# Kernel optimization log

Hardware: AMD Instinct MI355X
Metric: run time of the kernel (lower is better)

Reference implementation:

```python
import jax, jax.numpy as jnp
import numpy as np

KERNEL = 31
GROUPS = 8
EPS = 1e-5


def mha1d(x, Wq, Wk, Wv, rel):
    """Sliding-window multi-head attention (MutliHeadAttention1D).
    x: [b, s, in_f]; Wq/Wk/Wv: [out_f, in_f] (torch Linear layout); rel: [1, out_f, KERNEL].
    Returns (out [b, s, out_f], attn [b, s, GROUPS, KERNEL])."""
    b, s, _ = x.shape
    out_f = Wq.shape[0]
    d = out_f // GROUPS
    pad = (KERNEL - 1) // 2
    xp = jnp.pad(x, ((0, 0), (pad, pad), (0, 0)))
    q = jnp.einsum('bsf,of->bso', x, Wq)          # [b, s, out_f]
    k = jnp.einsum('bsf,of->bso', xp, Wk)         # [b, s+2*pad, out_f]
    v = jnp.einsum('bsf,of->bso', xp, Wv)
    # unfold: window index [s, KERNEL]
    idx = jnp.arange(s)[:, None] + jnp.arange(KERNEL)[None, :]
    kw = jnp.swapaxes(k[:, idx], 2, 3) + rel       # [b, s, out_f, KERNEL]
    vw = jnp.swapaxes(v[:, idx], 2, 3)             # [b, s, out_f, KERNEL]
    kw = kw.reshape(b, s, GROUPS, d, KERNEL)
    vw = vw.reshape(b, s, GROUPS, d, KERNEL)
    qh = q.reshape(b, s, GROUPS, d, 1)
    energy = jnp.sum(qh * kw, axis=-2, keepdims=True)   # [b, s, g, 1, K]
    attn = jax.nn.softmax(energy, axis=-1)               # [b, s, g, 1, K]
    out = jnp.sum(attn * vw, axis=-1).reshape(b, s, out_f)
    return out, attn[:, :, :, 0, :]


def layer_norm(x, g, b):
    mu = jnp.mean(x, axis=-1, keepdims=True)
    var = jnp.mean(jnp.square(x - mu), axis=-1, keepdims=True)
    return (x - mu) / jnp.sqrt(var + EPS) * g + b


def setup_inputs() -> dict:
    key = jax.random.key(0)
    ks = jax.random.split(key, 20)
    in_f, mc, out_f = 229, 48, 88
    d = {}
    d['spec'] = jax.random.normal(ks[0], (8, 8192, in_f), dtype=jnp.float32)
    # onset attention block (in 229 -> 48)
    d['Wq1'] = jax.random.normal(ks[1], (mc, in_f), dtype=jnp.float32) * 0.1
    d['Wk1'] = jax.random.normal(ks[2], (mc, in_f), dtype=jnp.float32) * 0.1
    d['Wv1'] = jax.random.normal(ks[3], (mc, in_f), dtype=jnp.float32) * 0.1
    d['rel1'] = jax.random.normal(ks[4], (1, mc, KERNEL), dtype=jnp.float32)
    d['ln1_g'] = jnp.ones((mc,), jnp.float32)
    d['ln1_b'] = jnp.zeros((mc,), jnp.float32)
    d['Wo'] = jax.random.normal(ks[5], (out_f, mc), dtype=jnp.float32) * 0.1
    d['bo'] = jnp.zeros((out_f,), jnp.float32)
    # frame attention block (in 48+88=136 -> 48)
    in2 = mc + out_f
    d['Wq2'] = jax.random.normal(ks[6], (mc, in2), dtype=jnp.float32) * 0.1
    d['Wk2'] = jax.random.normal(ks[7], (mc, in2), dtype=jnp.float32) * 0.1
    d['Wv2'] = jax.random.normal(ks[8], (mc, in2), dtype=jnp.float32) * 0.1
    d['rel2'] = jax.random.normal(ks[9], (1, mc, KERNEL), dtype=jnp.float32)
    d['ln2_g'] = jnp.ones((mc,), jnp.float32)
    d['ln2_b'] = jnp.zeros((mc,), jnp.float32)
    d['Wf'] = jax.random.normal(ks[10], (out_f, mc), dtype=jnp.float32) * 0.1
    d['bf'] = jnp.zeros((out_f,), jnp.float32)
    return d


def reference(spec, Wq1, Wk1, Wv1, rel1, ln1_g, ln1_b, Wo, bo,
              Wq2, Wk2, Wv2, rel2, ln2_g, ln2_b, Wf, bf):
    x, a = mha1d(spec, Wq1, Wk1, Wv1, rel1)
    x = layer_norm(x, ln1_g, ln1_b)
    onset_pred = jax.nn.sigmoid(jnp.einsum('bsm,om->bso', x, Wo) + bo)
    x = jnp.concatenate((onset_pred, x), axis=-1)
    x, _ = mha1d(x, Wq2, Wk2, Wv2, rel2)
    x = layer_norm(x, ln2_g, ln2_b)
    frame_pred = jax.nn.sigmoid(jnp.einsum('bsm,om->bso', x, Wf) + bf)
    return frame_pred, onset_pred, a
```

## Files before the change

### kernel.cpp

```cpp
#include <hip/hip_runtime.h>
#include <math.h>

namespace {

constexpr int B_   = 8;
constexpr int S_   = 8192;
constexpr int NROW = B_ * S_;
constexpr int MC   = 48;
constexpr int OF   = 88;
constexpr int KW   = 31;
constexpr int F1   = 229;
constexpr int F2   = 136;

typedef __attribute__((ext_vector_type(8))) short bf16x8;
typedef __attribute__((ext_vector_type(4))) float f32x4;

__device__ inline unsigned short f2bf(float v) {
    unsigned u = __float_as_uint(v);
    unsigned r = (u + 0x7FFFu + ((u >> 16) & 1u)) >> 16;
    return (unsigned short)r;
}
__device__ inline float bf2f(unsigned short b) {
    return __uint_as_float((unsigned)b << 16);
}
__device__ inline unsigned pack2(unsigned short a, unsigned short b) {
    return (unsigned)a | ((unsigned)b << 16);
}

__global__ void wprep_kernel(const float* __restrict__ Wq,
                             const float* __restrict__ Wk,
                             const float* __restrict__ Wv,
                             int K, int nch, unsigned short* __restrict__ out) {
    int idx = blockIdx.x * 256 + threadIdx.x;
    int kpad = nch * 32;
    int total = 144 * kpad;
    if (idx >= total) return;
    int oc = idx / kpad;
    int kg = idx - oc * kpad;
    int c  = kg >> 5, kk = kg & 31;
    float val = 0.f;
    if (kg < K) {
        const float* W = (oc < 48) ? Wq : (oc < 96 ? Wk : Wv);
        int ocl = (oc < 48) ? oc : (oc < 96 ? oc - 48 : oc - 96);
        val = W[ocl * K + kg];
    }
    unsigned short h = f2bf(val);
    unsigned short l = f2bf(val - bf2f(h));
    size_t base = (size_t)c * 16384 + (size_t)oc * 56 + kk;
    out[base]        = h;
    out[base + 8192] = l;
}

__global__ void woprep_kernel(const float* __restrict__ W,
                              unsigned short* __restrict__ out) {
    int idx = blockIdx.x * 256 + threadIdx.x;
    if (idx >= 96 * 64) return;
    int n = idx >> 6, k = idx & 63;
    float val = (n < OF && k < MC) ? W[n * MC + k] : 0.f;
    unsigned short h = f2bf(val);
    unsigned short l = f2bf(val - bf2f(h));
    out[idx]        = h;
    out[6144 + idx] = l;
}

template<int K, int NCH>
__global__ __launch_bounds__(256, 4) void proj_mfma(
    const float* __restrict__ x,
    const unsigned short* __restrict__ wbuf,
    float* __restrict__ qo, float* __restrict__ ko, float* __restrict__ vo)
{
    __shared__ __attribute__((aligned(16))) unsigned short Ah[64 * 56];
    __shared__ __attribute__((aligned(16))) unsigned short Al[64 * 56];
    __shared__ __attribute__((aligned(16))) unsigned short Bblk[16384];

    const int tid  = threadIdx.x;
    const int row0 = blockIdx.x * 64;
    const int lane = tid & 63;
    const int wm   = tid >> 6;
    const int lr   = lane & 15;
    const int ak   = (lane >> 4) * 8;
    const int arow = wm * 16 + lr;

    f32x4 acc[9];
    #pragma unroll
    for (int nt = 0; nt < 9; ++nt) acc[nt] = f32x4{0.f, 0.f, 0.f, 0.f};

    for (int c = 0; c < NCH; ++c) {
        {
            const uint4* src = (const uint4*)(wbuf + (size_t)c * 16384);
            uint4* dst = (uint4*)Bblk;
            #pragma unroll
            for (int i = 0; i < 8; ++i)
                dst[tid + 256 * i] = src[tid + 256 * i];
        }
        const int kc = c * 32;
        #pragma unroll
        for (int i = 0; i < 4; ++i) {
            int idx = tid + 256 * i;
            int r   = idx >> 4;
            int k2  = (idx & 15) * 2;
            int kg  = kc + k2;
            const float* xr = x + (size_t)(row0 + r) * K;
            float v0 = (kg     < K) ? xr[kg]     : 0.f;
            float v1 = (kg + 1 < K) ? xr[kg + 1] : 0.f;
            unsigned short h0 = f2bf(v0), h1 = f2bf(v1);
            unsigned short l0 = f2bf(v0 - bf2f(h0));
            unsigned short l1 = f2bf(v1 - bf2f(h1));
            *(unsigned*)&Ah[r * 56 + k2] = pack2(h0, h1);
            *(unsigned*)&Al[r * 56 + k2] = pack2(l0, l1);
        }
        __syncthreads();

        bf16x8 ah = *(const bf16x8*)&Ah[arow * 56 + ak];
        bf16x8 al = *(const bf16x8*)&Al[arow * 56 + ak];
        #pragma unroll
        for (int grp = 0; grp < 3; ++grp) {
            bf16x8 bh0 = *(const bf16x8*)&Bblk[((grp * 3 + 0) * 16 + lr) * 56 + ak];
            bf16x8 bl0 = *(const bf16x8*)&Bblk[8192 + ((grp * 3 + 0) * 16 + lr) * 56 + ak];
            bf16x8 bh1 = *(const bf16x8*)&Bblk[((grp * 3 + 1) * 16 + lr) * 56 + ak];
            bf16x8 bl1 = *(const bf16x8*)&Bblk[8192 + ((grp * 3 + 1) * 16 + lr) * 56 + ak];
            bf16x8 bh2 = *(const bf16x8*)&Bblk[((grp * 3 + 2) * 16 + lr) * 56 + ak];
            bf16x8 bl2 = *(const bf16x8*)&Bblk[8192 + ((grp * 3 + 2) * 16 + lr) * 56 + ak];
            acc[grp * 3 + 0] = __builtin_amdgcn_mfma_f32_16x16x32_bf16(ah, bh0, acc[grp * 3 + 0], 0, 0, 0);
            acc[grp * 3 + 0] = __builtin_amdgcn_mfma_f32_16x16x32_bf16(ah, bl0, acc[grp * 3 + 0], 0, 0, 0);
            acc[grp * 3 + 0] = __builtin_amdgcn_mfma_f32_16x16x32_bf16(al, bh0, acc[grp * 3 + 0], 0, 0, 0);
            acc[grp * 3 + 1] = __builtin_amdgcn_mfma_f32_16x16x32_bf16(ah, bh1, acc[grp * 3 + 1], 0, 0, 0);
            acc[grp * 3 + 1] = __builtin_amdgcn_mfma_f32_16x16x32_bf16(ah, bl1, acc[grp * 3 + 1], 0, 0, 0);
            acc[grp * 3 + 1] = __builtin_amdgcn_mfma_f32_16x16x32_bf16(al, bh1, acc[grp * 3 + 1], 0, 0, 0);
            acc[grp * 3 + 2] = __builtin_amdgcn_mfma_f32_16x16x32_bf16(ah, bh2, acc[grp * 3 + 2], 0, 0, 0);
            acc[grp * 3 + 2] = __builtin_amdgcn_mfma_f32_16x16x32_bf16(ah, bl2, acc[grp * 3 + 2], 0, 0, 0);
            acc[grp * 3 + 2] = __builtin_amdgcn_mfma_f32_16x16x32_bf16(al, bh2, acc[grp * 3 + 2], 0, 0, 0);
        }
        __syncthreads();
    }

    const int orow = row0 + wm * 16 + ((lane >> 4) << 2);
    #pragma unroll
    for (int nt = 0; nt < 9; ++nt) {
        float* dst = (nt < 3) ? qo : (nt < 6 ? ko : vo);
        int oc = (nt % 3) * 16 + lr;
        #pragma unroll
        for (int rg = 0; rg < 4; ++rg)
            dst[(size_t)(orow + rg) * MC + oc] = acc[nt][rg];
    }
}

template<bool FIRST>
__global__ __launch_bounds__(512, 6) void attn_core(
    const float* __restrict__ qb,
    const float* __restrict__ kb,
    const float* __restrict__ vb,
    const float* __restrict__ rel,
    const float* __restrict__ lng,
    const float* __restrict__ lnb,
    float* __restrict__ attn_out,
    float* __restrict__ x2)
{
    __shared__ __attribute__((aligned(16))) float ks[94 * 52];
    __shared__ __attribute__((aligned(16))) float vs[94 * 52];
    __shared__ __attribute__((aligned(16))) float relT[31 * 52];
    __shared__ float lngs[48], lnbs[48];

    const int tid = threadIdx.x;
    const int bid = ((blockIdx.x & 7) << 7) | (blockIdx.x >> 3);
    const int bb  = bid >> 7;
    const int st0 = (bid & 127) * 64;
    const size_t base = (size_t)bb * S_;

    for (int idx = tid; idx < 94 * 12; idx += 512) {
        int rr = idx / 12, c4 = idx - rr * 12;
        int si = st0 - 15 + rr;
        float4 k4 = {0.f, 0.f, 0.f, 0.f}, v4 = {0.f, 0.f, 0.f, 0.f};
        if (si >= 0 && si < S_) {
            k4 = *(const float4*)&kb[(base + si) * MC + c4 * 4];
            v4 = *(const float4*)&vb[(base + si) * MC + c4 * 4];
        }
        *(float4*)&ks[rr * 52 + c4 * 4] = k4;
        *(float4*)&vs[rr * 52 + c4 * 4] = v4;
    }
    for (int idx = tid; idx < MC * KW; idx += 512) {
        int c = idx / KW, j = idx - c * KW;
        relT[j * 52 + c] = rel[idx];
    }
    if (tid < 48) { lngs[tid] = lng[tid]; lnbs[tid] = lnb[tid]; }
    __syncthreads();

    const int rl  = tid >> 3;
    const int g   = tid & 7;
    const int ch0 = g * 6;
    const size_t grow = base + st0 + rl;

    const float* qr = qb + grow * MC + ch0;
    float2 q01 = *(const float2*)(qr);
    float2 q23 = *(const float2*)(qr + 2);
    float2 q45 = *(const float2*)(qr + 4);

    float e[KW];
    #pragma unroll
    for (int j = 0; j < KW; ++j) {
        const float* rp = &relT[j * 52 + ch0];
        float2 r01 = *(const float2*)(rp);
        float2 r23 = *(const float2*)(rp + 2);
        float2 r45 = *(const float2*)(rp + 4);
        e[j] = q01.x * r01.x + q01.y * r01.y + q23.x * r23.x
             + q23.y * r23.y + q45.x * r45.x + q45.y * r45.y;
    }
    float mx = -1e30f;
    #pragma unroll
    for (int j = 0; j < KW; ++j) {
        const float* kp = &ks[(rl + j) * 52 + ch0];
        float2 k01 = *(const float2*)(kp);
        float2 k23 = *(const float2*)(kp + 2);
        float2 k45 = *(const float2*)(kp + 4);
        float s = e[j] + q01.x * k01.x + q01.y * k01.y + q23.x * k23.x
                       + q23.y * k23.y + q45.x * k45.x + q45.y * k45.y;
        e[j] = s;
        mx = fmaxf(mx, s);
    }
    float den = 0.f;
    #pragma unroll
    for (int j = 0; j < KW; ++j) { float t = __expf(e[j] - mx); e[j] = t; den += t; }
    float rden = 1.f / den;

    float o0 = 0.f, o1 = 0.f, o2 = 0.f, o3 = 0.f, o4 = 0.f, o5 = 0.f;
    float* aout = FIRST ? (attn_out + (grow * 8 + g) * KW) : nullptr;
    #pragma unroll
    for (int j = 0; j < KW; ++j) {
        float aw = e[j] * rden;
        if constexpr (FIRST) aout[j] = aw;
        const float* vp = &vs[(rl + j) * 52 + ch0];
        float2 v01 = *(const float2*)(vp);
        float2 v23 = *(const float2*)(vp + 2);
        float2 v45 = *(const float2*)(vp + 4);
        o0 += aw * v01.x; o1 += aw * v01.y; o2 += aw * v23.x;
        o3 += aw * v23.y; o4 += aw * v45.x; o5 += aw * v45.y;
    }

    float sum = o0 + o1 + o2 + o3 + o4 + o5;
    sum += __shfl_xor(sum, 1, 8);
    sum += __shfl_xor(sum, 2, 8);
    sum += __shfl_xor(sum, 4, 8);
    float mu = sum * (1.f / 48.f);
    float d0 = o0 - mu, d1 = o1 - mu, d2 = o2 - mu, d3 = o3 - mu, d4 = o4 - mu, d5 = o5 - mu;
    float vr = d0*d0 + d1*d1 + d2*d2 + d3*d3 + d4*d4 + d5*d5;
    vr += __shfl_xor(vr, 1, 8);
    vr += __shfl_xor(vr, 2, 8);
    vr += __shfl_xor(vr, 4, 8);
    float rstd = rsqrtf(vr * (1.f / 48.f) + 1e-5f);

    float* xp = x2 + grow * F2 + OF + ch0;
    *(float2*)(xp)     = float2{d0 * rstd * lngs[ch0]     + lnbs[ch0],
                                d1 * rstd * lngs[ch0 + 1] + lnbs[ch0 + 1]};
    *(float2*)(xp + 2) = float2{d2 * rstd * lngs[ch0 + 2] + lnbs[ch0 + 2],
                                d3 * rstd * lngs[ch0 + 3] + lnbs[ch0 + 3]};
    *(float2*)(xp + 4) = float2{d4 * rstd * lngs[ch0 + 4] + lnbs[ch0 + 4],
                                d5 * rstd * lngs[ch0 + 5] + lnbs[ch0 + 5]};
}

template<bool FIRST>
__global__ __launch_bounds__(256, 4) void pred_gemm(
    const float* x2,
    const unsigned short* __restrict__ wop,
    const float* __restrict__ bo,
    float* __restrict__ pred,
    float* x2w)
{
    __shared__ __attribute__((aligned(16))) unsigned short yh[64 * 72];
    __shared__ __attribute__((aligned(16))) unsigned short yl[64 * 72];
    __shared__ float bosL[96];

    const int tid  = threadIdx.x;
    const int row0 = blockIdx.x * 64;

    for (int idx = tid; idx < 768; idx += 256) {
        int r = idx / 12, c4 = idx - r * 12;
        float4 v4 = *(const float4*)&x2[(size_t)(row0 + r) * F2 + OF + c4 * 4];
        unsigned short h0 = f2bf(v4.x), h1 = f2bf(v4.y), h2 = f2bf(v4.z), h3 = f2bf(v4.w);
        unsigned short l0 = f2bf(v4.x - bf2f(h0)), l1 = f2bf(v4.y - bf2f(h1));
        unsigned short l2 = f2bf(v4.z - bf2f(h2)), l3 = f2bf(v4.w - bf2f(h3));
        *(uint2*)&yh[r * 72 + c4 * 4] = uint2{pack2(h0, h1), pack2(h2, h3)};
        *(uint2*)&yl[r * 72 + c4 * 4] = uint2{pack2(l0, l1), pack2(l2, l3)};
    }
    for (int idx = tid; idx < 384; idx += 256) {
        int r = idx / 6, u = idx - r * 6;
        *(uint2*)&yh[r * 72 + 48 + u * 4] = uint2{0u, 0u};
        *(uint2*)&yl[r * 72 + 48 + u * 4] = uint2{0u, 0u};
    }
    if (tid < 96) bosL[tid] = (tid < OF) ? bo[tid] : 0.f;
    __syncthreads();

    const int l   = tid & 63;
    const int w   = tid >> 6;
    const int lr  = l & 15;
    const int lk8 = (l >> 4) * 8;

    const int arow = w * 16 + lr;
    bf16x8 ah0 = *(const bf16x8*)&yh[arow * 72 + lk8];
    bf16x8 al0 = *(const bf16x8*)&yl[arow * 72 + lk8];
    bf16x8 ah1 = *(const bf16x8*)&yh[arow * 72 + 32 + lk8];
    bf16x8 al1 = *(const bf16x8*)&yl[arow * 72 + 32 + lk8];

    const int rowo = row0 + w * 16 + ((l >> 4) << 2);
    #pragma unroll
    for (int nt = 0; nt < 6; ++nt) {
        int ncol = nt * 16 + lr;
        bf16x8 bh0 = *(const bf16x8*)&wop[(size_t)ncol * 64 + lk8];
        bf16x8 bl0 = *(const bf16x8*)&wop[6144 + (size_t)ncol * 64 + lk8];
        bf16x8 bh1 = *(const bf16x8*)&wop[(size_t)ncol * 64 + 32 + lk8];
        bf16x8 bl1 = *(const bf16x8*)&wop[6144 + (size_t)ncol * 64 + 32 + lk8];
        f32x4 oacc = f32x4{0.f, 0.f, 0.f, 0.f};
        oacc = __builtin_amdgcn_mfma_f32_16x16x32_bf16(ah0, bh0, oacc, 0, 0, 0);
        oacc = __builtin_amdgcn_mfma_f32_16x16x32_bf16(ah0, bl0, oacc, 0, 0, 0);
        oacc = __builtin_amdgcn_mfma_f32_16x16x32_bf16(al0, bh0, oacc, 0, 0, 0);
        oacc = __builtin_amdgcn_mfma_f32_16x16x32_bf16(ah1, bh1, oacc, 0, 0, 0);
        oacc = __builtin_amdgcn_mfma_f32_16x16x32_bf16(ah1, bl1, oacc, 0, 0, 0);
        oacc = __builtin_amdgcn_mfma_f32_16x16x32_bf16(al1, bh1, oacc, 0, 0, 0);
        if (ncol < OF) {
            float bias = bosL[ncol];
            #pragma unroll
            for (int rg = 0; rg < 4; ++rg) {
                float s  = oacc[rg] + bias;
                float sg = 1.f / (1.f + __expf(-s));
                size_t row = (size_t)(rowo + rg);
                pred[row * OF + ncol] = sg;
                if constexpr (FIRST) x2w[row * F2 + ncol] = sg;
            }
        }
    }
}

}

extern "C" void kernel_launch(void* const* d_in, const int* in_sizes, int n_in,
                              void* d_out, int out_size, void* d_ws, size_t ws_size,
                              hipStream_t stream) {
    const float* spec = (const float*)d_in[0];
    const float* Wq1  = (const float*)d_in[1];
    const float* Wk1  = (const float*)d_in[2];
    const float* Wv1  = (const float*)d_in[3];
    const float* rel1 = (const float*)d_in[4];
    const float* ln1g = (const float*)d_in[5];
    const float* ln1b = (const float*)d_in[6];
    const float* Wo   = (const float*)d_in[7];
    const float* bo   = (const float*)d_in[8];
    const float* Wq2  = (const float*)d_in[9];
    const float* Wk2  = (const float*)d_in[10];
    const float* Wv2  = (const float*)d_in[11];
    const float* rel2 = (const float*)d_in[12];
    const float* ln2g = (const float*)d_in[13];
    const float* ln2b = (const float*)d_in[14];
    const float* Wf   = (const float*)d_in[15];
    const float* bf_  = (const float*)d_in[16];

    float* outf   = (float*)d_out;
    float* frame  = outf;
    float* onset  = outf + (size_t)NROW * OF;
    float* attn_a = outf + (size_t)2 * NROW * OF;

    float* wsf = (float*)d_ws;
    float* q1 = wsf;
    float* k1 = q1 + (size_t)NROW * MC;
    float* v1 = k1 + (size_t)NROW * MC;
    float* x2 = v1 + (size_t)NROW * MC;
    unsigned short* wbuf1 = (unsigned short*)(x2 + (size_t)NROW * F2);
    unsigned short* wbuf2 = wbuf1 + (size_t)8 * 16384;
    unsigned short* woP1  = wbuf2 + (size_t)5 * 16384;
    unsigned short* woP2  = woP1 + 2 * 6144;

    wprep_kernel<<<(144 * 8 * 32 + 255) / 256, 256, 0, stream>>>(Wq1, Wk1, Wv1, F1, 8, wbuf1);
    wprep_kernel<<<(144 * 5 * 32 + 255) / 256, 256, 0, stream>>>(Wq2, Wk2, Wv2, F2, 5, wbuf2);
    woprep_kernel<<<24, 256, 0, stream>>>(Wo, woP1);
    woprep_kernel<<<24, 256, 0, stream>>>(Wf, woP2);

    proj_mfma<F1, 8><<<NROW / 64, 256, 0, stream>>>(spec, wbuf1, q1, k1, v1);
    attn_core<true><<<NROW / 64, 512, 0, stream>>>(q1, k1, v1, rel1, ln1g, ln1b,
                                                   attn_a, x2);
    pred_gemm<true><<<NROW / 64, 256, 0, stream>>>(x2, woP1, bo, onset, x2);
    proj_mfma<F2, 5><<<NROW / 64, 256, 0, stream>>>(x2, wbuf2, q1, k1, v1);
    attn_core<false><<<NROW / 64, 512, 0, stream>>>(q1, k1, v1, rel2, ln2g, ln2b,
                                                    nullptr, x2);
    pred_gemm<false><<<NROW / 64, 256, 0, stream>>>(x2, woP2, bf_, frame, nullptr);
}
```

Measured before the change: 202.4 us.

## Load projection operands directly into registers, dropping LDS staging and barriers

The QKV projection kernel no longer stages the x tile and weight chunk through shared memory. Each lane now reads its own 8 x values and its bf16 hi/lo weight fragments straight from global memory, and the weight prep writes a fragment-major layout so each lane's 8 values sit contiguously. This removes the LDS copies and the two __syncthreads per K-chunk. In exchange the weights are re-fetched from global/L2 by every wave, x loads are strided per lane, and register pressure rises, so the occupancy hint drops from 4 to 3 blocks.

```diff
diff --git a/kernel.cpp b/kernel.cpp
--- a/kernel.cpp
+++ b/kernel.cpp
@@ -46,9 +46,9 @@
     }
     unsigned short h = f2bf(val);
     unsigned short l = f2bf(val - bf2f(h));
-    size_t base = (size_t)c * 16384 + (size_t)oc * 56 + kk;
+    size_t base = (size_t)c * 9216 + (size_t)((kk >> 3) * 144 + oc) * 8 + (kk & 7);
     out[base]        = h;
-    out[base + 8192] = l;
+    out[base + 4608] = l;
 }
 
 __global__ void woprep_kernel(const float* __restrict__ W,
@@ -64,77 +64,61 @@
 }
 
 template<int K, int NCH>
-__global__ __launch_bounds__(256, 4) void proj_mfma(
+__global__ __launch_bounds__(256, 3) void proj_mfma(
     const float* __restrict__ x,
     const unsigned short* __restrict__ wbuf,
     float* __restrict__ qo, float* __restrict__ ko, float* __restrict__ vo)
 {
-    __shared__ __attribute__((aligned(16))) unsigned short Ah[64 * 56];
-    __shared__ __attribute__((aligned(16))) unsigned short Al[64 * 56];
-    __shared__ __attribute__((aligned(16))) unsigned short Bblk[16384];
-
     const int tid  = threadIdx.x;
     const int row0 = blockIdx.x * 64;
     const int lane = tid & 63;
     const int wm   = tid >> 6;
     const int lr   = lane & 15;
-    const int ak   = (lane >> 4) * 8;
+    const int hig  = lane >> 4;
     const int arow = wm * 16 + lr;
 
+    const float* xrow = x + (size_t)(row0 + arow) * K;
+    const unsigned short* wl = wbuf + (size_t)(hig * 144 + lr) * 8;
+
     f32x4 acc[9];
     #pragma unroll
     for (int nt = 0; nt < 9; ++nt) acc[nt] = f32x4{0.f, 0.f, 0.f, 0.f};
 
     for (int c = 0; c < NCH; ++c) {
-        {
-            const uint4* src = (const uint4*)(wbuf + (size_t)c * 16384);
-            uint4* dst = (uint4*)Bblk;
-            #pragma unroll
-            for (int i = 0; i < 8; ++i)
-                dst[tid + 256 * i] = src[tid + 256 * i];
-        }
-        const int kc = c * 32;
-        #pragma unroll
-        for (int i = 0; i < 4; ++i) {
-            int idx = tid + 256 * i;
-            int r   = idx >> 4;
-            int k2  = (idx & 15) * 2;
-            int kg  = kc + k2;
-            const float* xr = x + (size_t)(row0 + r) * K;
-            float v0 = (kg     < K) ? xr[kg]     : 0.f;
-            float v1 = (kg + 1 < K) ? xr[kg + 1] : 0.f;
-            unsigned short h0 = f2bf(v0), h1 = f2bf(v1);
-            unsigned short l0 = f2bf(v0 - bf2f(h0));
-            unsigned short l1 = f2bf(v1 - bf2f(h1));
-            *(unsigned*)&Ah[r * 56 + k2] = pack2(h0, h1);
-            *(unsigned*)&Al[r * 56 + k2] = pack2(l0, l1);
-        }
-        __syncthreads();
-
-        bf16x8 ah = *(const bf16x8*)&Ah[arow * 56 + ak];
-        bf16x8 al = *(const bf16x8*)&Al[arow * 56 + ak];
-        #pragma unroll
-        for (int grp = 0; grp < 3; ++grp) {
-            bf16x8 bh0 = *(const bf16x8*)&Bblk[((grp * 3 + 0) * 16 + lr) * 56 + ak];
-            bf16x8 bl0 = *(const bf16x8*)&Bblk[8192 + ((grp * 3 + 0) * 16 + lr) * 56 + ak];
-            bf16x8 bh1 = *(const bf16x8*)&Bblk[((grp * 3 + 1) * 16 + lr) * 56 + ak];
-            bf16x8 bl1 = *(const bf16x8*)&Bblk[8192 + ((grp * 3 + 1) * 16 + lr) * 56 + ak];
-            bf16x8 bh2 = *(const bf16x8*)&Bblk[((grp * 3 + 2) * 16 + lr) * 56 + ak];
-            bf16x8 bl2 = *(const bf16x8*)&Bblk[8192 + ((grp * 3 + 2) * 16 + lr) * 56 + ak];
-            acc[grp * 3 + 0] = __builtin_amdgcn_mfma_f32_16x16x32_bf16(ah, bh0, acc[grp * 3 + 0], 0, 0, 0);
-            acc[grp * 3 + 0] = __builtin_amdgcn_mfma_f32_16x16x32_bf16(ah, bl0, acc[grp * 3 + 0], 0, 0, 0);
-            acc[grp * 3 + 0] = __builtin_amdgcn_mfma_f32_16x16x32_bf16(al, bh0, acc[grp * 3 + 0], 0, 0, 0);
-            acc[grp * 3 + 1] = __builtin_amdgcn_mfma_f32_16x16x32_bf16(ah, bh1, acc[grp * 3 + 1], 0, 0, 0);
-            acc[grp * 3 + 1] = __builtin_amdgcn_mfma_f32_16x16x32_bf16(ah, bl1, acc[grp * 3 + 1], 0, 0, 0);
-            acc[grp * 3 + 1] = __builtin_amdgcn_mfma_f32_16x16x32_bf16(al, bh1, acc[grp * 3 + 1], 0, 0, 0);
-            acc[grp * 3 + 2] = __builtin_amdgcn_mfma_f32_16x16x32_bf16(ah, bh2, acc[grp * 3 + 2], 0, 0, 0);
-            acc[grp * 3 + 2] = __builtin_amdgcn_mfma_f32_16x16x32_bf16(ah, bl2, acc[grp * 3 + 2], 0, 0, 0);
-            acc[grp * 3 + 2] = __builtin_amdgcn_mfma_f32_16x16x32_bf16(al, bh2, acc[grp * 3 + 2], 0, 0, 0);
-        }
-        __syncthreads();
-    }
-
-    const int orow = row0 + wm * 16 + ((lane >> 4) << 2);
+        const int k0 = c * 32 + hig * 8;
+        float av[8];
+        #pragma unroll
+        for (int u = 0; u < 8; ++u)
+            av[u] = (k0 + u < K) ? xrow[k0 + u] : 0.f;
+
+        const unsigned short* wc = wl + (size_t)c * 9216;
+        bf16x8 bh[9], bl[9];
+        #pragma unroll
+        for (int nt = 0; nt < 9; ++nt) {
+            bh[nt] = *(const bf16x8*)&wc[nt * 128];
+            bl[nt] = *(const bf16x8*)&wc[4608 + nt * 128];
+        }
+        __builtin_amdgcn_sched_barrier(0);
+
+        union { bf16x8 v; unsigned u[4]; } ah, al;
+        #pragma unroll
+        for (int p = 0; p < 4; ++p) {
+            unsigned short h0 = f2bf(av[2 * p]);
+            unsigned short h1 = f2bf(av[2 * p + 1]);
+            ah.u[p] = pack2(h0, h1);
+            al.u[p] = pack2(f2bf(av[2 * p]     - bf2f(h0)),
+                            f2bf(av[2 * p + 1] - bf2f(h1)));
+        }
+
+        #pragma unroll
+        for (int nt = 0; nt < 9; ++nt) {
+            acc[nt] = __builtin_amdgcn_mfma_f32_16x16x32_bf16(ah.v, bh[nt], acc[nt], 0, 0, 0);
+            acc[nt] = __builtin_amdgcn_mfma_f32_16x16x32_bf16(ah.v, bl[nt], acc[nt], 0, 0, 0);
+            acc[nt] = __builtin_amdgcn_mfma_f32_16x16x32_bf16(al.v, bh[nt], acc[nt], 0, 0, 0);
+        }
+    }
+
+    const int orow = row0 + wm * 16 + (hig << 2);
     #pragma unroll
     for (int nt = 0; nt < 9; ++nt) {
         float* dst = (nt < 3) ? qo : (nt < 6 ? ko : vo);
@@ -363,8 +347,8 @@
     float* v1 = k1 + (size_t)NROW * MC;
     float* x2 = v1 + (size_t)NROW * MC;
     unsigned short* wbuf1 = (unsigned short*)(x2 + (size_t)NROW * F2);
-    unsigned short* wbuf2 = wbuf1 + (size_t)8 * 16384;
-    unsigned short* woP1  = wbuf2 + (size_t)5 * 16384;
+    unsigned short* wbuf2 = wbuf1 + (size_t)8 * 9216;
+    unsigned short* woP1  = wbuf2 + (size_t)5 * 9216;
     unsigned short* woP2  = woP1 + 2 * 6144;
 
     wprep_kernel<<<(144 * 8 * 32 + 255) / 256, 256, 0, stream>>>(Wq1, Wk1, Wv1, F1, 8, wbuf1);
```

New measurement: 192.5 us. 1.05x faster.
